# Kernel optimization log

Measured on AMD Instinct MI355X. Metric: run time of the kernel, lower is better.

Reference implementation:

```python
import jax, jax.numpy as jnp
import numpy as np

DIM = 768
N_HEADS = 12
HEAD_DIM = DIM // N_HEADS
MAX_REL = 3  # hardcoded in the module


def setup_inputs() -> dict:
    key = jax.random.key(0)
    ks = jax.random.split(key, 10)
    B, L = 4, 1024
    def xavier(k, shape):
        fan_in, fan_out = shape[-2], shape[-1]
        a = jnp.sqrt(6.0 / (fan_in + fan_out))
        return jax.random.uniform(k, shape, jnp.float32, -a, a)
    return {
        "query": jax.random.normal(ks[0], (B, L, DIM), jnp.float32),
        "key":   jax.random.normal(ks[1], (B, L, DIM), jnp.float32),
        "value": jax.random.normal(ks[2], (B, L, DIM), jnp.float32),
        "Wq": xavier(ks[3], (DIM, DIM)),
        "Wk": xavier(ks[4], (DIM, DIM)),
        "Wv": xavier(ks[5], (DIM, DIM)),
        "Wproj": xavier(ks[6], (DIM, DIM)),
        "b_proj": jnp.zeros((DIM,), jnp.float32),
        "rel_k_table": xavier(ks[7], (2 * MAX_REL + 1, HEAD_DIM)),
        "rel_v_table": xavier(ks[8], (2 * MAX_REL + 1, HEAD_DIM)),
    }


def _rel_embed(table, len_q, len_k):
    # [len_q, len_k, head_dim] gathered from clipped relative distances
    dist = jnp.arange(len_k)[None, :] - jnp.arange(len_q)[:, None]
    idx = jnp.clip(dist, -MAX_REL, MAX_REL) + MAX_REL
    return table[idx]


def reference(query, key, value, Wq, Wk, Wv, Wproj, b_proj, rel_k_table, rel_v_table):
    B, Lq, _ = query.shape
    Lk = key.shape[1]
    H, hd = N_HEADS, HEAD_DIM
    scale = hd ** (-0.5)

    q = query @ Wq.T                      # [B, Lq, D]
    k = key @ Wk.T                        # [B, Lk, D]
    v = value @ Wv.T                      # [B, Lk, D]

    qh = q.reshape(B, Lq, H, hd).transpose(0, 2, 1, 3)   # [B,H,Lq,hd]
    kh = k.reshape(B, Lk, H, hd).transpose(0, 2, 1, 3)
    vh = v.reshape(B, Lk, H, hd).transpose(0, 2, 1, 3)

    # content-content scores
    attn1 = jnp.einsum('bhqd,bhkd->bhqk', qh, kh)
    # content-relative-position scores
    rk = _rel_embed(rel_k_table, Lq, Lk)                  # [Lq,Lk,hd]
    attn2 = jnp.einsum('bhqd,qkd->bhqk', qh, rk)
    # NOTE: original code DIVIDES by scale (= hd**-0.5), i.e. multiplies by sqrt(hd)
    attn = (attn1 + attn2) / scale
    attn = jax.nn.softmax(attn, axis=-1)                  # [B,H,Lq,Lk]

    w1 = jnp.einsum('bhqk,bhkd->bhqd', attn, vh)
    rv = _rel_embed(rel_v_table, Lq, Lk)                  # [Lq,Lk,hd]
    w2 = jnp.einsum('bhqk,qkd->bhqd', attn, rv)

    x = (w1 + w2).transpose(0, 2, 1, 3).reshape(B, Lq, H * hd)
    x = x @ Wproj.T + b_proj
    return (x, attn)
```

## Files before the change

### kernel.cpp

```cpp
#include <hip/hip_runtime.h>

#define DIMM 768
#define NH 12
#define HD 64
#define LSEQ 1024
#define BATCH 4
#define NXE 3145728
#define NWE 589824

typedef __bf16 bf16x8 __attribute__((ext_vector_type(8)));
typedef float f32x4 __attribute__((ext_vector_type(4)));
typedef unsigned short u16;

static __device__ __forceinline__ u16 f2bf(float f) {
  unsigned u = __builtin_bit_cast(unsigned, f);
  u += 0x7fffu + ((u >> 16) & 1u);
  return (u16)(u >> 16);
}
static __device__ __forceinline__ float bf2f(u16 h) {
  unsigned u = ((unsigned)h) << 16;
  return __builtin_bit_cast(float, u);
}
static __device__ __forceinline__ bf16x8 ld8bf(const u16* p) {
  uint4 u = *(const uint4*)p;
  return __builtin_bit_cast(bf16x8, u);
}
#define MFMA(a, b, c) __builtin_amdgcn_mfma_f32_16x16x32_bf16(a, b, c, 0, 0, 0)
#define GLL(g, s)                                                      \
  __builtin_amdgcn_global_load_lds(                                    \
      (const __attribute__((address_space(1))) void*)(g),              \
      (__attribute__((address_space(3))) void*)(s), 16, 0, 0)

__global__ __launch_bounds__(256) void convert(
    const float* __restrict__ q_in, const float* __restrict__ k_in,
    const float* __restrict__ v_in, const float* __restrict__ Wq,
    const float* __restrict__ Wk, const float* __restrict__ Wv,
    const float* __restrict__ Wp, u16* __restrict__ AqH, u16* __restrict__ AqL,
    u16* __restrict__ AkH, u16* __restrict__ AkL, u16* __restrict__ Av,
    u16* __restrict__ WqH, u16* __restrict__ WqL, u16* __restrict__ WkH,
    u16* __restrict__ WkL, u16* __restrict__ Wvr, u16* __restrict__ Wpr) {
  long i = ((long)blockIdx.x * 256 + threadIdx.x) * 4;
  const float* src;
  u16 *dh, *dl = nullptr;
  long off;
  if (i < NXE) { src = q_in; dh = AqH; dl = AqL; off = i; }
  else if (i < 2L * NXE) { src = k_in; dh = AkH; dl = AkL; off = i - NXE; }
  else if (i < 3L * NXE) { src = v_in; dh = Av; off = i - 2L * NXE; }
  else {
    long j = i - 3L * NXE;
    int which = (int)(j / NWE);
    off = j % NWE;
    if (which == 0) { src = Wq; dh = WqH; dl = WqL; }
    else if (which == 1) { src = Wk; dh = WkH; dl = WkL; }
    else if (which == 2) { src = Wv; dh = Wvr; }
    else { src = Wp; dh = Wpr; }
  }
  float4 v = *(const float4*)(src + off);
  ushort4 h;
  h.x = f2bf(v.x); h.y = f2bf(v.y); h.z = f2bf(v.z); h.w = f2bf(v.w);
  *(ushort4*)(dh + off) = h;
  if (dl) {
    ushort4 lo;
    lo.x = f2bf(v.x - bf2f(h.x)); lo.y = f2bf(v.y - bf2f(h.y));
    lo.z = f2bf(v.z - bf2f(h.z)); lo.w = f2bf(v.w - bf2f(h.w));
    *(ushort4*)(dl + off) = lo;
  }
}

__global__ __launch_bounds__(256, 3) void gemm_multi(
    int mode0, const u16* __restrict__ AqH, const u16* __restrict__ AqL,
    const u16* __restrict__ AkH, const u16* __restrict__ AkL,
    const u16* __restrict__ Av, const u16* __restrict__ WqH,
    const u16* __restrict__ WqL, const u16* __restrict__ WkH,
    const u16* __restrict__ WkL, const u16* __restrict__ Wvr,
    const u16* __restrict__ Wpr, const u16* __restrict__ wbuf,
    u16* __restrict__ qhi, u16* __restrict__ qlo, u16* __restrict__ khi,
    u16* __restrict__ klo, u16* __restrict__ vT, float* __restrict__ outp,
    const float* __restrict__ bias) {
  __shared__ u16 sAh[128 * 32], sAl[128 * 32];
  __shared__ u16 sBh[128 * 32], sBl[128 * 32];
  const int mode = mode0 + blockIdx.z;
  const u16 *Ah, *Al = nullptr, *Bh, *Bl = nullptr;
  if (mode == 0) { Ah = AqH; Al = AqL; Bh = WqH; Bl = WqL; }
  else if (mode == 1) { Ah = AkH; Al = AkL; Bh = WkH; Bl = WkL; }
  else if (mode == 2) { Ah = Av; Bh = Wvr; }
  else { Ah = wbuf; Bh = Wpr; }
  const int t = threadIdx.x, w = t >> 6, l = t & 63;
  const int quad = l >> 4, l15 = l & 15;
  const int m0 = blockIdx.x * 128, n0 = blockIdx.y * 128;
  const int wm = (w >> 1) * 64, wn = (w & 1) * 64;
  const int srow = t >> 2, scol = (t & 3) * 8;
  const u16* gA = Ah + (m0 + srow) * DIMM + scol;
  const u16* gB = Bh + (n0 + srow) * DIMM + scol;
  u16* lA = sAh + w * 512;
  u16* lB = sBh + w * 512;
  f32x4 acc[4][4] = {};
  if (mode < 2) {
    const u16* gAl = Al + (m0 + srow) * DIMM + scol;
    const u16* gBl = Bl + (n0 + srow) * DIMM + scol;
    u16* lAl = sAl + w * 512;
    u16* lBl = sBl + w * 512;
    for (int k0 = 0; k0 < DIMM; k0 += 32) {
      GLL(gA + k0, lA);
      GLL(gA + 64 * DIMM + k0, lA + 2048);
      GLL(gAl + k0, lAl);
      GLL(gAl + 64 * DIMM + k0, lAl + 2048);
      GLL(gB + k0, lB);
      GLL(gB + 64 * DIMM + k0, lB + 2048);
      GLL(gBl + k0, lBl);
      GLL(gBl + 64 * DIMM + k0, lBl + 2048);
      __syncthreads();
      bf16x8 ah[4], bh[4], xl[4];
#pragma unroll
      for (int i = 0; i < 4; ++i)
        ah[i] = __builtin_bit_cast(
            bf16x8, *(const uint4*)(sAh + (wm + i * 16 + l15) * 32 + quad * 8));
#pragma unroll
      for (int j = 0; j < 4; ++j)
        bh[j] = __builtin_bit_cast(
            bf16x8, *(const uint4*)(sBh + (wn + j * 16 + l15) * 32 + quad * 8));
#pragma unroll
      for (int i = 0; i < 4; ++i)
#pragma unroll
        for (int j = 0; j < 4; ++j) acc[i][j] = MFMA(ah[i], bh[j], acc[i][j]);
#pragma unroll
      for (int i = 0; i < 4; ++i)
        xl[i] = __builtin_bit_cast(
            bf16x8, *(const uint4*)(sAl + (wm + i * 16 + l15) * 32 + quad * 8));
#pragma unroll
      for (int i = 0; i < 4; ++i)
#pragma unroll
        for (int j = 0; j < 4; ++j) acc[i][j] = MFMA(xl[i], bh[j], acc[i][j]);
#pragma unroll
      for (int j = 0; j < 4; ++j)
        xl[j] = __builtin_bit_cast(
            bf16x8, *(const uint4*)(sBl + (wn + j * 16 + l15) * 32 + quad * 8));
#pragma unroll
      for (int i = 0; i < 4; ++i)
#pragma unroll
        for (int j = 0; j < 4; ++j) acc[i][j] = MFMA(ah[i], xl[j], acc[i][j]);
      __syncthreads();
    }
  } else {
    for (int k0 = 0; k0 < DIMM; k0 += 32) {
      GLL(gA + k0, lA);
      GLL(gA + 64 * DIMM + k0, lA + 2048);
      GLL(gB + k0, lB);
      GLL(gB + 64 * DIMM + k0, lB + 2048);
      __syncthreads();
      bf16x8 ah[4], bh[4];
#pragma unroll
      for (int i = 0; i < 4; ++i)
        ah[i] = __builtin_bit_cast(
            bf16x8, *(const uint4*)(sAh + (wm + i * 16 + l15) * 32 + quad * 8));
#pragma unroll
      for (int j = 0; j < 4; ++j)
        bh[j] = __builtin_bit_cast(
            bf16x8, *(const uint4*)(sBh + (wn + j * 16 + l15) * 32 + quad * 8));
#pragma unroll
      for (int i = 0; i < 4; ++i)
#pragma unroll
        for (int j = 0; j < 4; ++j) acc[i][j] = MFMA(ah[i], bh[j], acc[i][j]);
      __syncthreads();
    }
  }
  u16* oh = (mode == 0) ? qhi : khi;
  u16* ol = (mode == 0) ? qlo : klo;
#pragma unroll
  for (int i = 0; i < 4; ++i)
#pragma unroll
    for (int j = 0; j < 4; ++j)
#pragma unroll
      for (int r = 0; r < 4; ++r) {
        int grow = m0 + wm + i * 16 + quad * 4 + r;
        int gcol = n0 + wn + j * 16 + l15;
        float c = acc[i][j][r];
        int b = grow >> 10, ll = grow & 1023, h = gcol >> 6, d = gcol & 63;
        if (mode < 2) {
          int idx = ((b * NH + h) * LSEQ + ll) * HD + d;
          u16 hi = f2bf(c);
          oh[idx] = hi;
          ol[idx] = f2bf(c - bf2f(hi));
        } else if (mode == 2) {
          vT[((b * NH + h) * HD + d) * LSEQ + ll] = f2bf(c);
        } else {
          outp[grow * DIMM + gcol] = c + bias[gcol];
        }
      }
}

__global__ __launch_bounds__(256, 3) void attn_core(
    const u16* __restrict__ qhi, const u16* __restrict__ qlo,
    const u16* __restrict__ khi, const u16* __restrict__ klo,
    const u16* __restrict__ vT, const float* __restrict__ relk,
    const float* __restrict__ relv, float* __restrict__ attn_out,
    u16* __restrict__ wbuf) {
  __shared__ __align__(16) u16 uni[16 * 1032];
  __shared__ float qrel[16][7];
  __shared__ float arel[16][7];
  __shared__ float rvt[7][64];
  __shared__ float red[4][16][4];

  const int qt = blockIdx.x, h = blockIdx.y, b = blockIdx.z;
  const int q0 = qt * 16;
  const int tid = threadIdx.x, wave = tid >> 6, lane = tid & 63;
  const int quad = lane >> 4, l15 = lane & 15;
  const int bhd = b * NH + h;

  for (int t = tid; t < 7 * HD; t += 256) rvt[t >> 6][t & 63] = relv[t];
  if (tid < 112) {
    int q = tid / 7, rr = tid % 7;
    const u16* qp = qhi + (bhd * LSEQ + q0 + q) * HD;
    const u16* lp = qlo + (bhd * LSEQ + q0 + q) * HD;
    const float* tp = relk + rr * HD;
    float s = 0.f;
#pragma unroll
    for (int d8 = 0; d8 < HD; d8 += 8) {
      uint4 uh = *(const uint4*)(qp + d8);
      uint4 ul = *(const uint4*)(lp + d8);
      float4 t0 = *(const float4*)(tp + d8);
      float4 t1 = *(const float4*)(tp + d8 + 4);
      unsigned hh[4] = {uh.x, uh.y, uh.z, uh.w};
      unsigned lv[4] = {ul.x, ul.y, ul.z, ul.w};
      float tv[8] = {t0.x, t0.y, t0.z, t0.w, t1.x, t1.y, t1.z, t1.w};
#pragma unroll
      for (int m = 0; m < 4; ++m) {
        s += (bf2f((u16)(hh[m] & 0xffff)) + bf2f((u16)(lv[m] & 0xffff))) * tv[2 * m];
        s += (bf2f((u16)(hh[m] >> 16)) + bf2f((u16)(lv[m] >> 16))) * tv[2 * m + 1];
      }
    }
    qrel[q][rr] = s;
    arel[q][rr] = 0.f;
  }

  f32x4 sc[16];
  {
    const int qbase = (bhd * LSEQ + q0 + l15) * HD + quad * 8;
    bf16x8 ah0 = ld8bf(qhi + qbase);
    bf16x8 ah1 = ld8bf(qhi + qbase + 32);
    bf16x8 al0 = ld8bf(qlo + qbase);
    bf16x8 al1 = ld8bf(qlo + qbase + 32);
    const int r = tid >> 3;
    const int cg = (tid & 7) ^ (r & 7);
    const u16* gh = khi + (bhd * LSEQ + r) * HD + cg * 8;
    const u16* gl = klo + (bhd * LSEQ + r) * HD + cg * 8;
    u16* sb = uni + wave * 512;
    const int rowA = wave * 16 + l15;
    const int sw = rowA & 7;
    const int s0 = (rowA * 8 + (quad ^ sw)) * 8;
    const int s1 = (rowA * 8 + ((quad + 4) ^ sw)) * 8;
    for (int c = 0; c < 16; ++c) {
      const u16* ghc = gh + c * 64 * HD;
      const u16* glc = gl + c * 64 * HD;
      GLL(ghc, sb);
      GLL(ghc + 32 * HD, sb + 2048);
      GLL(glc, sb + 4096);
      GLL(glc + 32 * HD, sb + 6144);
      __syncthreads();
      bf16x8 kh0 = ld8bf(uni + s0);
      bf16x8 kh1 = ld8bf(uni + s1);
      bf16x8 kl0 = ld8bf(uni + 4096 + s0);
      bf16x8 kl1 = ld8bf(uni + 4096 + s1);
      f32x4 e = {}, f = {};
      e = MFMA(ah0, kh0, e);
      f = MFMA(ah1, kh1, f);
      e = MFMA(ah0, kl0, e);
      f = MFMA(ah1, kl1, f);
      e = MFMA(al0, kh0, e);
      f = MFMA(al1, kh1, f);
      sc[c] = e + f;
      __syncthreads();
    }
  }

  const int colbase = wave * 16 + l15;
  const int dbase = colbase - q0 - quad * 4;
  float mrow[4] = {-3.4e38f, -3.4e38f, -3.4e38f, -3.4e38f};
#pragma unroll
  for (int c = 0; c < 16; ++c)
#pragma unroll
    for (int r = 0; r < 4; ++r) {
      int d = dbase + c * 64 - r;
      int ri = d < -3 ? 0 : (d > 3 ? 6 : d + 3);
      float s = (sc[c][r] + qrel[quad * 4 + r][ri]) * 8.0f;
      sc[c][r] = s;
      mrow[r] = fmaxf(mrow[r], s);
    }
#pragma unroll
  for (int m = 1; m <= 8; m <<= 1)
#pragma unroll
    for (int r = 0; r < 4; ++r) mrow[r] = fmaxf(mrow[r], __shfl_xor(mrow[r], m));
  if (l15 < 4) {
    float mv = l15 == 0 ? mrow[0] : l15 == 1 ? mrow[1] : l15 == 2 ? mrow[2] : mrow[3];
    red[0][quad * 4 + l15][wave] = mv;
  }
  __syncthreads();
  float mx[4];
#pragma unroll
  for (int r = 0; r < 4; ++r) {
    int row = quad * 4 + r;
    mx[r] = fmaxf(fmaxf(red[0][row][0], red[0][row][1]),
                  fmaxf(red[0][row][2], red[0][row][3]));
  }

  float sum[4] = {}, s0a[4] = {}, s6a[4] = {};
#pragma unroll
  for (int c = 0; c < 16; ++c)
#pragma unroll
    for (int r = 0; r < 4; ++r) {
      float e = __expf(sc[c][r] - mx[r]);
      sc[c][r] = e;
      int d = dbase + c * 64 - r;
      sum[r] += e;
      if (d <= -3) s0a[r] += e;
      if (d >= 3) s6a[r] += e;
    }
#pragma unroll
  for (int m = 1; m <= 8; m <<= 1)
#pragma unroll
    for (int r = 0; r < 4; ++r) {
      sum[r] += __shfl_xor(sum[r], m);
      s0a[r] += __shfl_xor(s0a[r], m);
      s6a[r] += __shfl_xor(s6a[r], m);
    }
  if (l15 < 4) {
    int row = quad * 4 + l15;
    float sv = l15 == 0 ? sum[0] : l15 == 1 ? sum[1] : l15 == 2 ? sum[2] : sum[3];
    float a0 = l15 == 0 ? s0a[0] : l15 == 1 ? s0a[1] : l15 == 2 ? s0a[2] : s0a[3];
    float a6 = l15 == 0 ? s6a[0] : l15 == 1 ? s6a[1] : l15 == 2 ? s6a[2] : s6a[3];
    red[1][row][wave] = sv;
    red[2][row][wave] = a0;
    red[3][row][wave] = a6;
  }
  __syncthreads();
  float rn[4];
#pragma unroll
  for (int r = 0; r < 4; ++r) {
    int row = quad * 4 + r;
    float s = red[1][row][0] + red[1][row][1] + red[1][row][2] + red[1][row][3];
    rn[r] = 1.0f / s;
    if (wave == 0 && l15 == 0) {
      float t0 = red[2][row][0] + red[2][row][1] + red[2][row][2] + red[2][row][3];
      float t6 = red[3][row][0] + red[3][row][1] + red[3][row][2] + red[3][row][3];
      arel[row][0] = t0 * rn[r];
      arel[row][6] = t6 * rn[r];
    }
  }

#pragma unroll
  for (int c = 0; c < 16; ++c) {
    int col = colbase + c * 64;
#pragma unroll
    for (int r = 0; r < 4; ++r) {
      int row = quad * 4 + r;
      float p = sc[c][r] * rn[r];
      uni[row * 1032 + col] = f2bf(p);
      int d = dbase + c * 64 - r;
      if (d >= -2 && d <= 2) arel[row][d + 3] = p;
    }
  }
  __syncthreads();

  {
    float* aob = attn_out + ((size_t)(bhd * LSEQ + q0)) * LSEQ;
#pragma unroll
    for (int row = 0; row < 16; ++row) {
      uint2 u = *(const uint2*)&uni[row * 1032 + tid * 4];
      float4 f = {bf2f((u16)(u.x & 0xffff)), bf2f((u16)(u.x >> 16)),
                  bf2f((u16)(u.y & 0xffff)), bf2f((u16)(u.y >> 16))};
      *(float4*)(aob + row * LSEQ + tid * 4) = f;
    }
  }

  {
    const u16* vb = vT + (bhd * HD + wave * 16 + l15) * LSEQ;
    f32x4 acc = {};
#pragma unroll 4
    for (int kk = 0; kk < LSEQ; kk += 32) {
      int ak = kk + quad * 8;
      bf16x8 aP = __builtin_bit_cast(bf16x8, *(const uint4*)&uni[l15 * 1032 + ak]);
      bf16x8 bV = ld8bf(vb + ak);
      acc = MFMA(aP, bV, acc);
    }
    const int col = wave * 16 + l15;
#pragma unroll
    for (int r = 0; r < 4; ++r) {
      int row = quad * 4 + r;
      float w2 = 0.f;
#pragma unroll
      for (int t = 0; t < 7; ++t) w2 += arel[row][t] * rvt[t][col];
      wbuf[(b * LSEQ + q0 + row) * DIMM + h * HD + col] = f2bf(acc[r] + w2);
    }
  }
}

extern "C" void kernel_launch(void* const* d_in, const int* in_sizes, int n_in,
                              void* d_out, int out_size, void* d_ws, size_t ws_size,
                              hipStream_t stream) {
  const float* q_in = (const float*)d_in[0];
  const float* k_in = (const float*)d_in[1];
  const float* v_in = (const float*)d_in[2];
  const float* Wq = (const float*)d_in[3];
  const float* Wk = (const float*)d_in[4];
  const float* Wv = (const float*)d_in[5];
  const float* Wp = (const float*)d_in[6];
  const float* bias = (const float*)d_in[7];
  const float* relk = (const float*)d_in[8];
  const float* relv = (const float*)d_in[9];
  float* out = (float*)d_out;

  u16* p = (u16*)d_ws;
  u16 *AqH = p, *AqL = AqH + NXE, *AkH = AqL + NXE, *AkL = AkH + NXE,
      *Av = AkL + NXE;
  u16 *WqH = Av + NXE, *WqL = WqH + NWE, *WkH = WqL + NWE, *WkL = WkH + NWE,
      *Wvr = WkL + NWE, *Wpr = Wvr + NWE;
  u16 *qhi = Wpr + NWE, *qlo = qhi + NXE, *khi = qlo + NXE, *klo = khi + NXE,
      *vT = klo + NXE, *wbuf = vT + NXE;

  convert<<<(3 * NXE + 4 * NWE) / 1024, 256, 0, stream>>>(
      q_in, k_in, v_in, Wq, Wk, Wv, Wp, AqH, AqL, AkH, AkL, Av, WqH, WqL, WkH,
      WkL, Wvr, Wpr);
  gemm_multi<<<dim3(32, 6, 3), 256, 0, stream>>>(
      0, AqH, AqL, AkH, AkL, Av, WqH, WqL, WkH, WkL, Wvr, Wpr, wbuf, qhi, qlo,
      khi, klo, vT, out, bias);
  attn_core<<<dim3(64, NH, BATCH), 256, 0, stream>>>(
      qhi, qlo, khi, klo, vT, relk, relv, out + NXE, wbuf);
  gemm_multi<<<dim3(32, 6, 1), 256, 0, stream>>>(
      3, AqH, AqL, AkH, AkL, Av, WqH, WqL, WkH, WkL, Wvr, Wpr, wbuf, qhi, qlo,
      khi, klo, vT, out, bias);
}
```

Measured before the change: 435.0 us.

## Process 32 query rows per attention block and double-buffer K tile loads

Each attention block now handles 32 query rows instead of 16. Every K tile loaded into shared memory therefore feeds two query sub-tiles, and each V fragment is reused for two accumulators. K tile loads are double-buffered across the two halves of the shared buffer so the next tile's global-to-LDS copy overlaps the current MFMAs, which also drops one barrier per iteration. The cost is twice the score registers and LDS per block, half as many blocks, and launch bounds lowered to 2 blocks per SM, so occupancy falls.

Measured after the change: 501.9 us. +15.4%, slower.

```diff
diff --git a/kernel.cpp b/kernel.cpp
--- a/kernel.cpp
+++ b/kernel.cpp
@@ -189,26 +189,26 @@
       }
 }
 
-__global__ __launch_bounds__(256, 3) void attn_core(
+__global__ __launch_bounds__(256, 2) void attn_core(
     const u16* __restrict__ qhi, const u16* __restrict__ qlo,
     const u16* __restrict__ khi, const u16* __restrict__ klo,
     const u16* __restrict__ vT, const float* __restrict__ relk,
     const float* __restrict__ relv, float* __restrict__ attn_out,
     u16* __restrict__ wbuf) {
-  __shared__ __align__(16) u16 uni[16 * 1032];
-  __shared__ float qrel[16][7];
-  __shared__ float arel[16][7];
+  __shared__ __align__(16) u16 uni[32 * 1032];
+  __shared__ float qrel[32][7];
+  __shared__ float arel[32][7];
   __shared__ float rvt[7][64];
-  __shared__ float red[4][16][4];
+  __shared__ float red[4][32][4];
 
   const int qt = blockIdx.x, h = blockIdx.y, b = blockIdx.z;
-  const int q0 = qt * 16;
+  const int q0 = qt * 32;
   const int tid = threadIdx.x, wave = tid >> 6, lane = tid & 63;
   const int quad = lane >> 4, l15 = lane & 15;
   const int bhd = b * NH + h;
 
   for (int t = tid; t < 7 * HD; t += 256) rvt[t >> 6][t & 63] = relv[t];
-  if (tid < 112) {
+  if (tid < 224) {
     int q = tid / 7, rr = tid % 7;
     const u16* qp = qhi + (bhd * LSEQ + q0 + q) * HD;
     const u16* lp = qlo + (bhd * LSEQ + q0 + q) * HD;
@@ -233,138 +233,181 @@
     arel[q][rr] = 0.f;
   }
 
-  f32x4 sc[16];
+  f32x4 sc[2][16];
   {
-    const int qbase = (bhd * LSEQ + q0 + l15) * HD + quad * 8;
-    bf16x8 ah0 = ld8bf(qhi + qbase);
-    bf16x8 ah1 = ld8bf(qhi + qbase + 32);
-    bf16x8 al0 = ld8bf(qlo + qbase);
-    bf16x8 al1 = ld8bf(qlo + qbase + 32);
+    bf16x8 ah[2][2], al[2][2];
+#pragma unroll
+    for (int qq = 0; qq < 2; ++qq) {
+      const int qbase = (bhd * LSEQ + q0 + qq * 16 + l15) * HD + quad * 8;
+      ah[qq][0] = ld8bf(qhi + qbase);
+      ah[qq][1] = ld8bf(qhi + qbase + 32);
+      al[qq][0] = ld8bf(qlo + qbase);
+      al[qq][1] = ld8bf(qlo + qbase + 32);
+    }
     const int r = tid >> 3;
     const int cg = (tid & 7) ^ (r & 7);
     const u16* gh = khi + (bhd * LSEQ + r) * HD + cg * 8;
     const u16* gl = klo + (bhd * LSEQ + r) * HD + cg * 8;
-    u16* sb = uni + wave * 512;
     const int rowA = wave * 16 + l15;
     const int sw = rowA & 7;
     const int s0 = (rowA * 8 + (quad ^ sw)) * 8;
     const int s1 = (rowA * 8 + ((quad + 4) ^ sw)) * 8;
+    {
+      u16* sb = uni + wave * 512;
+      GLL(gh, sb);
+      GLL(gh + 32 * HD, sb + 2048);
+      GLL(gl, sb + 4096);
+      GLL(gl + 32 * HD, sb + 6144);
+    }
     for (int c = 0; c < 16; ++c) {
-      const u16* ghc = gh + c * 64 * HD;
-      const u16* glc = gl + c * 64 * HD;
-      GLL(ghc, sb);
-      GLL(ghc + 32 * HD, sb + 2048);
-      GLL(glc, sb + 4096);
-      GLL(glc + 32 * HD, sb + 6144);
       __syncthreads();
-      bf16x8 kh0 = ld8bf(uni + s0);
-      bf16x8 kh1 = ld8bf(uni + s1);
-      bf16x8 kl0 = ld8bf(uni + 4096 + s0);
-      bf16x8 kl1 = ld8bf(uni + 4096 + s1);
-      f32x4 e = {}, f = {};
-      e = MFMA(ah0, kh0, e);
-      f = MFMA(ah1, kh1, f);
-      e = MFMA(ah0, kl0, e);
-      f = MFMA(ah1, kl1, f);
-      e = MFMA(al0, kh0, e);
-      f = MFMA(al1, kh1, f);
-      sc[c] = e + f;
-      __syncthreads();
+      const int cur = (c & 1) * 8192;
+      if (c < 15) {
+        u16* sb = uni + ((c + 1) & 1) * 8192 + wave * 512;
+        const u16* ghc = gh + (c + 1) * 64 * HD;
+        const u16* glc = gl + (c + 1) * 64 * HD;
+        GLL(ghc, sb);
+        GLL(ghc + 32 * HD, sb + 2048);
+        GLL(glc, sb + 4096);
+        GLL(glc + 32 * HD, sb + 6144);
+      }
+      bf16x8 kh0 = ld8bf(uni + cur + s0);
+      bf16x8 kh1 = ld8bf(uni + cur + s1);
+      bf16x8 kl0 = ld8bf(uni + cur + 4096 + s0);
+      bf16x8 kl1 = ld8bf(uni + cur + 4096 + s1);
+#pragma unroll
+      for (int qq = 0; qq < 2; ++qq) {
+        f32x4 e = {}, f = {};
+        e = MFMA(ah[qq][0], kh0, e);
+        f = MFMA(ah[qq][1], kh1, f);
+        e = MFMA(ah[qq][0], kl0, e);
+        f = MFMA(ah[qq][1], kl1, f);
+        e = MFMA(al[qq][0], kh0, e);
+        f = MFMA(al[qq][1], kh1, f);
+        sc[qq][c] = e + f;
+      }
     }
   }
 
   const int colbase = wave * 16 + l15;
-  const int dbase = colbase - q0 - quad * 4;
-  float mrow[4] = {-3.4e38f, -3.4e38f, -3.4e38f, -3.4e38f};
+  float mrow[2][4] = {{-3.4e38f, -3.4e38f, -3.4e38f, -3.4e38f},
+                      {-3.4e38f, -3.4e38f, -3.4e38f, -3.4e38f}};
 #pragma unroll
   for (int c = 0; c < 16; ++c)
 #pragma unroll
+    for (int qq = 0; qq < 2; ++qq)
+#pragma unroll
+      for (int r = 0; r < 4; ++r) {
+        int row = qq * 16 + quad * 4 + r;
+        int d = colbase + c * 64 - q0 - row;
+        int ri = d < -3 ? 0 : (d > 3 ? 6 : d + 3);
+        float s = (sc[qq][c][r] + qrel[row][ri]) * 8.0f;
+        sc[qq][c][r] = s;
+        mrow[qq][r] = fmaxf(mrow[qq][r], s);
+      }
+#pragma unroll
+  for (int m = 1; m <= 8; m <<= 1)
+#pragma unroll
+    for (int qq = 0; qq < 2; ++qq)
+#pragma unroll
+      for (int r = 0; r < 4; ++r)
+        mrow[qq][r] = fmaxf(mrow[qq][r], __shfl_xor(mrow[qq][r], m));
+  if (l15 < 4) {
+#pragma unroll
+    for (int qq = 0; qq < 2; ++qq) {
+      float mv = l15 == 0 ? mrow[qq][0] : l15 == 1 ? mrow[qq][1]
+                 : l15 == 2 ? mrow[qq][2] : mrow[qq][3];
+      red[0][qq * 16 + quad * 4 + l15][wave] = mv;
+    }
+  }
+  __syncthreads();
+  float mx[2][4];
+#pragma unroll
+  for (int qq = 0; qq < 2; ++qq)
+#pragma unroll
     for (int r = 0; r < 4; ++r) {
-      int d = dbase + c * 64 - r;
-      int ri = d < -3 ? 0 : (d > 3 ? 6 : d + 3);
-      float s = (sc[c][r] + qrel[quad * 4 + r][ri]) * 8.0f;
-      sc[c][r] = s;
-      mrow[r] = fmaxf(mrow[r], s);
-    }
+      int row = qq * 16 + quad * 4 + r;
+      mx[qq][r] = fmaxf(fmaxf(red[0][row][0], red[0][row][1]),
+                        fmaxf(red[0][row][2], red[0][row][3]));
+    }
+
+  float sum[2][4] = {}, s0a[2][4] = {}, s6a[2][4] = {};
+#pragma unroll
+  for (int c = 0; c < 16; ++c)
+#pragma unroll
+    for (int qq = 0; qq < 2; ++qq)
+#pragma unroll
+      for (int r = 0; r < 4; ++r) {
+        int row = qq * 16 + quad * 4 + r;
+        float e = __expf(sc[qq][c][r] - mx[qq][r]);
+        sc[qq][c][r] = e;
+        int d = colbase + c * 64 - q0 - row;
+        sum[qq][r] += e;
+        if (d <= -3) s0a[qq][r] += e;
+        if (d >= 3) s6a[qq][r] += e;
+      }
 #pragma unroll
   for (int m = 1; m <= 8; m <<= 1)
 #pragma unroll
-    for (int r = 0; r < 4; ++r) mrow[r] = fmaxf(mrow[r], __shfl_xor(mrow[r], m));
+    for (int qq = 0; qq < 2; ++qq)
+#pragma unroll
+      for (int r = 0; r < 4; ++r) {
+        sum[qq][r] += __shfl_xor(sum[qq][r], m);
+        s0a[qq][r] += __shfl_xor(s0a[qq][r], m);
+        s6a[qq][r] += __shfl_xor(s6a[qq][r], m);
+      }
   if (l15 < 4) {
-    float mv = l15 == 0 ? mrow[0] : l15 == 1 ? mrow[1] : l15 == 2 ? mrow[2] : mrow[3];
-    red[0][quad * 4 + l15][wave] = mv;
+#pragma unroll
+    for (int qq = 0; qq < 2; ++qq) {
+      int row = qq * 16 + quad * 4 + l15;
+      float sv = l15 == 0 ? sum[qq][0] : l15 == 1 ? sum[qq][1]
+                 : l15 == 2 ? sum[qq][2] : sum[qq][3];
+      float a0 = l15 == 0 ? s0a[qq][0] : l15 == 1 ? s0a[qq][1]
+                 : l15 == 2 ? s0a[qq][2] : s0a[qq][3];
+      float a6 = l15 == 0 ? s6a[qq][0] : l15 == 1 ? s6a[qq][1]
+                 : l15 == 2 ? s6a[qq][2] : s6a[qq][3];
+      red[1][row][wave] = sv;
+      red[2][row][wave] = a0;
+      red[3][row][wave] = a6;
+    }
   }
   __syncthreads();
-  float mx[4];
-#pragma unroll
-  for (int r = 0; r < 4; ++r) {
-    int row = quad * 4 + r;
-    mx[r] = fmaxf(fmaxf(red[0][row][0], red[0][row][1]),
-                  fmaxf(red[0][row][2], red[0][row][3]));
-  }
-
-  float sum[4] = {}, s0a[4] = {}, s6a[4] = {};
-#pragma unroll
-  for (int c = 0; c < 16; ++c)
+  float rn[2][4];
+#pragma unroll
+  for (int qq = 0; qq < 2; ++qq)
 #pragma unroll
     for (int r = 0; r < 4; ++r) {
-      float e = __expf(sc[c][r] - mx[r]);
-      sc[c][r] = e;
-      int d = dbase + c * 64 - r;
-      sum[r] += e;
-      if (d <= -3) s0a[r] += e;
-      if (d >= 3) s6a[r] += e;
-    }
-#pragma unroll
-  for (int m = 1; m <= 8; m <<= 1)
-#pragma unroll
-    for (int r = 0; r < 4; ++r) {
-      sum[r] += __shfl_xor(sum[r], m);
-      s0a[r] += __shfl_xor(s0a[r], m);
-      s6a[r] += __shfl_xor(s6a[r], m);
-    }
-  if (l15 < 4) {
-    int row = quad * 4 + l15;
-    float sv = l15 == 0 ? sum[0] : l15 == 1 ? sum[1] : l15 == 2 ? sum[2] : sum[3];
-    float a0 = l15 == 0 ? s0a[0] : l15 == 1 ? s0a[1] : l15 == 2 ? s0a[2] : s0a[3];
-    float a6 = l15 == 0 ? s6a[0] : l15 == 1 ? s6a[1] : l15 == 2 ? s6a[2] : s6a[3];
-    red[1][row][wave] = sv;
-    red[2][row][wave] = a0;
-    red[3][row][wave] = a6;
-  }
-  __syncthreads();
-  float rn[4];
-#pragma unroll
-  for (int r = 0; r < 4; ++r) {
-    int row = quad * 4 + r;
-    float s = red[1][row][0] + red[1][row][1] + red[1][row][2] + red[1][row][3];
-    rn[r] = 1.0f / s;
-    if (wave == 0 && l15 == 0) {
-      float t0 = red[2][row][0] + red[2][row][1] + red[2][row][2] + red[2][row][3];
-      float t6 = red[3][row][0] + red[3][row][1] + red[3][row][2] + red[3][row][3];
-      arel[row][0] = t0 * rn[r];
-      arel[row][6] = t6 * rn[r];
-    }
-  }
+      int row = qq * 16 + quad * 4 + r;
+      float s = red[1][row][0] + red[1][row][1] + red[1][row][2] + red[1][row][3];
+      rn[qq][r] = 1.0f / s;
+      if (wave == 0 && l15 == 0) {
+        float t0 = red[2][row][0] + red[2][row][1] + red[2][row][2] + red[2][row][3];
+        float t6 = red[3][row][0] + red[3][row][1] + red[3][row][2] + red[3][row][3];
+        arel[row][0] = t0 * rn[qq][r];
+        arel[row][6] = t6 * rn[qq][r];
+      }
+    }
 
 #pragma unroll
   for (int c = 0; c < 16; ++c) {
     int col = colbase + c * 64;
 #pragma unroll
-    for (int r = 0; r < 4; ++r) {
-      int row = quad * 4 + r;
-      float p = sc[c][r] * rn[r];
-      uni[row * 1032 + col] = f2bf(p);
-      int d = dbase + c * 64 - r;
-      if (d >= -2 && d <= 2) arel[row][d + 3] = p;
-    }
+    for (int qq = 0; qq < 2; ++qq)
+#pragma unroll
+      for (int r = 0; r < 4; ++r) {
+        int row = qq * 16 + quad * 4 + r;
+        float p = sc[qq][c][r] * rn[qq][r];
+        uni[row * 1032 + col] = f2bf(p);
+        int d = col - q0 - row;
+        if (d >= -2 && d <= 2) arel[row][d + 3] = p;
+      }
   }
   __syncthreads();
 
   {
     float* aob = attn_out + ((size_t)(bhd * LSEQ + q0)) * LSEQ;
 #pragma unroll
-    for (int row = 0; row < 16; ++row) {
+    for (int row = 0; row < 32; ++row) {
       uint2 u = *(const uint2*)&uni[row * 1032 + tid * 4];
       float4 f = {bf2f((u16)(u.x & 0xffff)), bf2f((u16)(u.x >> 16)),
                   bf2f((u16)(u.y & 0xffff)), bf2f((u16)(u.y >> 16))};
@@ -374,23 +417,28 @@
 
   {
     const u16* vb = vT + (bhd * HD + wave * 16 + l15) * LSEQ;
-    f32x4 acc = {};
+    f32x4 acc[2] = {};
 #pragma unroll 4
     for (int kk = 0; kk < LSEQ; kk += 32) {
       int ak = kk + quad * 8;
-      bf16x8 aP = __builtin_bit_cast(bf16x8, *(const uint4*)&uni[l15 * 1032 + ak]);
       bf16x8 bV = ld8bf(vb + ak);
-      acc = MFMA(aP, bV, acc);
+      bf16x8 aP0 = __builtin_bit_cast(bf16x8, *(const uint4*)&uni[l15 * 1032 + ak]);
+      bf16x8 aP1 =
+          __builtin_bit_cast(bf16x8, *(const uint4*)&uni[(16 + l15) * 1032 + ak]);
+      acc[0] = MFMA(aP0, bV, acc[0]);
+      acc[1] = MFMA(aP1, bV, acc[1]);
     }
     const int col = wave * 16 + l15;
 #pragma unroll
-    for (int r = 0; r < 4; ++r) {
-      int row = quad * 4 + r;
-      float w2 = 0.f;
-#pragma unroll
-      for (int t = 0; t < 7; ++t) w2 += arel[row][t] * rvt[t][col];
-      wbuf[(b * LSEQ + q0 + row) * DIMM + h * HD + col] = f2bf(acc[r] + w2);
-    }
+    for (int qq = 0; qq < 2; ++qq)
+#pragma unroll
+      for (int r = 0; r < 4; ++r) {
+        int row = qq * 16 + quad * 4 + r;
+        float w2 = 0.f;
+#pragma unroll
+        for (int t = 0; t < 7; ++t) w2 += arel[row][t] * rvt[t][col];
+        wbuf[(b * LSEQ + q0 + row) * DIMM + h * HD + col] = f2bf(acc[qq][r] + w2);
+      }
   }
 }
 
@@ -423,7 +471,7 @@
   gemm_multi<<<dim3(32, 6, 3), 256, 0, stream>>>(
       0, AqH, AqL, AkH, AkL, Av, WqH, WqL, WkH, WkL, Wvr, Wpr, wbuf, qhi, qlo,
       khi, klo, vT, out, bias);
-  attn_core<<<dim3(64, NH, BATCH), 256, 0, stream>>>(
+  attn_core<<<dim3(32, NH, BATCH), 256, 0, stream>>>(
       qhi, qlo, khi, klo, vT, relk, relv, out + NXE, wbuf);
   gemm_multi<<<dim3(32, 6, 1), 256, 0, stream>>>(
       3, AqH, AqL, AkH, AkL, Av, WqH, WqL, WkH, WkL, Wvr, Wpr, wbuf, qhi, qlo,
```
